# Kernel tuning notes

Hardware: AMD Instinct MI355X
Metric: run time of the kernel (lower is better)

Reference implementation:

```python
import jax, jax.numpy as jnp
import numpy as np

D_MODEL = 2048
NUM_EXPERTS = 64
TOP_K = 2


def setup_inputs() -> dict:
    key = jax.random.key(0)
    kx, kw, kb = jax.random.split(key, 3)
    x = jax.random.normal(kx, (4, 4096, D_MODEL), dtype=jnp.float32)
    # nn.Linear(d_model, num_experts): weight [num_experts, d_model], bias [num_experts]
    bound = 1.0 / np.sqrt(D_MODEL)
    W = jax.random.uniform(kw, (NUM_EXPERTS, D_MODEL), minval=-bound, maxval=bound, dtype=jnp.float32)
    b = jax.random.uniform(kb, (NUM_EXPERTS,), minval=-bound, maxval=bound, dtype=jnp.float32)
    return {"x": x, "W": W, "b": b}


def reference(x, W, b):
    # Eval mode: no noise injection (self.training is False).
    logits = jnp.einsum('bsd,ed->bse', x, W) + b          # [B, S, E]
    raw_weights = jax.nn.softmax(logits, axis=-1)          # [B, S, E]
    top_k_weights, top_k_indices = jax.lax.top_k(raw_weights, TOP_K)  # [B, S, K]
    normalized = top_k_weights / jnp.sum(top_k_weights, axis=-1, keepdims=True)
    return normalized, top_k_indices
```

## Files before the change

kernel.cpp:

```cpp
#include <hip/hip_runtime.h>
#include <math.h>

#define DM 2048
#define NEXP 64
#define NTOK 16384
#define NSLICE 4
#define KSL (DM / NSLICE)
#define KC 32
#define NCH (KSL / KC)
#define MBLK 64
#define NBLK1 ((NTOK / MBLK) * NSLICE)
#define NKG (DM / KC)
#define WFRAG_BYTES (NKG * 12 * 1024)
#define PART_BYTES (NSLICE * NEXP * NTOK * 4)

typedef __attribute__((ext_vector_type(8))) short short8;
typedef __attribute__((ext_vector_type(4))) short short4v;
typedef __attribute__((ext_vector_type(4))) float f32x4;

__device__ __forceinline__ void split3t(float f, unsigned short& h,
                                        unsigned short& m, unsigned short& l) {
  unsigned u = __float_as_uint(f);
  h = (unsigned short)(u >> 16);
  float f1 = f - __uint_as_float(u & 0xFFFF0000u);
  unsigned u1 = __float_as_uint(f1);
  m = (unsigned short)(u1 >> 16);
  float f2 = f1 - __uint_as_float(u1 & 0xFFFF0000u);
  l = (unsigned short)(__float_as_uint(f2) >> 16);
}

__device__ __forceinline__ void split8(const f32x4& a0, const f32x4& a1,
                                       short8& h, short8& m, short8& l) {
  float v[8] = {a0[0], a0[1], a0[2], a0[3], a1[0], a1[1], a1[2], a1[3]};
#pragma unroll
  for (int j = 0; j < 8; ++j) {
    unsigned short hh, mm, ll;
    split3t(v[j], hh, mm, ll);
    h[j] = (short)hh; m[j] = (short)mm; l[j] = (short)ll;
  }
}

__global__ void convw_kernel(const float* __restrict__ W,
                             unsigned short* __restrict__ wfrag) {
  const int kg = blockIdx.x;
  const int lane = threadIdx.x & 63;
  const int nt = threadIdx.x >> 6;
  const int e = nt * 16 + (lane & 15);
  const int kpos = kg * 32 + (lane >> 4) * 8;
  const f32x4* wp = (const f32x4*)(W + (size_t)e * DM + kpos);
  f32x4 w0 = wp[0], w1 = wp[1];
  short8 h, m, l;
  split8(w0, w1, h, m, l);
  size_t base = ((size_t)(kg * 12 + nt) * 64 + lane) * 8;
  *(short8*)(wfrag + base) = h;
  *(short8*)(wfrag + base + (size_t)4 * 64 * 8) = m;
  *(short8*)(wfrag + base + (size_t)8 * 64 * 8) = l;
}

__global__ __launch_bounds__(256, 4)
void router_gemm(const float* __restrict__ x,
                 const unsigned short* __restrict__ wfrag,
                 float* __restrict__ part) {
  const int lane = threadIdx.x & 63;
  const int wv = threadIdx.x >> 6;
  const int col = lane & 15;
  const int quad = lane >> 4;
  const int tg = blockIdx.x >> 2;
  const int s = blockIdx.x & 3;
  const int tok0 = tg * MBLK;
  const int kg0 = s * NCH;

  const float* xp =
      x + (size_t)(tok0 + wv * 16 + col) * DM + s * KSL + quad * 8;
  const unsigned short* bb = wfrag + (size_t)lane * 8;

  f32x4 acc[4];
#pragma unroll
  for (int nt = 0; nt < 4; ++nt) acc[nt] = (f32x4){0.f, 0.f, 0.f, 0.f};

  f32x4 pa0 = ((const f32x4*)xp)[0];
  f32x4 pa1 = ((const f32x4*)xp)[1];
  f32x4 qa0 = ((const f32x4*)(xp + KC))[0];
  f32x4 qa1 = ((const f32x4*)(xp + KC))[1];

  short8 Bh = *(const short8*)(bb + (size_t)(kg0 * 12 + 0) * 512);
  short8 Bm = *(const short8*)(bb + (size_t)(kg0 * 12 + 4) * 512);
  short8 Bl = *(const short8*)(bb + (size_t)(kg0 * 12 + 8) * 512);

#pragma unroll
  for (int c = 0; c < NCH; ++c) {
    const int kg = kg0 + c;
    short8 ah, am, al;
    split8(pa0, pa1, ah, am, al);
    pa0 = qa0; pa1 = qa1;
    if (c + 2 < NCH) {
      const float* xn = xp + (size_t)(c + 2) * KC;
      qa0 = ((const f32x4*)xn)[0];
      qa1 = ((const f32x4*)xn)[1];
    }
#pragma unroll
    for (int nt = 0; nt < 4; ++nt) {
      short8 bh = Bh, bm = Bm, bl = Bl;
      const int nf = (nt < 3) ? (kg * 12 + nt + 1)
                              : ((c + 1 < NCH) ? (kg + 1) * 12 : -1);
      if (nf >= 0) {
        Bh = *(const short8*)(bb + (size_t)(nf + 0) * 512);
        Bm = *(const short8*)(bb + (size_t)(nf + 4) * 512);
        Bl = *(const short8*)(bb + (size_t)(nf + 8) * 512);
      }
      f32x4 cc = acc[nt];
      cc = __builtin_amdgcn_mfma_f32_16x16x32_bf16(ah, bh, cc, 0, 0, 0);
      cc = __builtin_amdgcn_mfma_f32_16x16x32_bf16(ah, bm, cc, 0, 0, 0);
      cc = __builtin_amdgcn_mfma_f32_16x16x32_bf16(am, bh, cc, 0, 0, 0);
      cc = __builtin_amdgcn_mfma_f32_16x16x32_bf16(ah, bl, cc, 0, 0, 0);
      cc = __builtin_amdgcn_mfma_f32_16x16x32_bf16(al, bh, cc, 0, 0, 0);
      cc = __builtin_amdgcn_mfma_f32_16x16x32_bf16(am, bm, cc, 0, 0, 0);
      acc[nt] = cc;
    }
  }

#pragma unroll
  for (int nt = 0; nt < 4; ++nt) {
    const size_t e = (size_t)(s * NEXP + nt * 16 + col);
    *(f32x4*)(part + e * NTOK + tok0 + wv * 16 + quad * 4) = acc[nt];
  }
}

__global__ __launch_bounds__(256, 4)
void router_reduce(const float* __restrict__ part,
                   const float* __restrict__ bias, float* __restrict__ out) {
  const int lane = threadIdx.x & 63;
  const int wv = threadIdx.x >> 6;
  const int q = lane >> 4;
  const int t = blockIdx.x * 64 + wv * 16 + (lane & 15);

  float v1 = -INFINITY, v2 = -INFINITY;
  int i1 = 0, i2 = 0;
#pragma unroll
  for (int e = 0; e < NEXP; ++e) {
    float p = part[(size_t)(q * NEXP + e) * NTOK + t];
    p += __shfl_xor(p, 16, 64);
    p += __shfl_xor(p, 32, 64);
    const float v = p + bias[e];
    const bool a = v > v1;
    const bool b = v > v2;
    const float nv2 = a ? v1 : (b ? v : v2);
    const int ni2 = a ? i1 : (b ? e : i2);
    v2 = nv2; i2 = ni2;
    i1 = a ? e : i1;
    v1 = a ? v : v1;
  }
  if (q == 0) {
    const float ex = expf(v2 - v1);
    const float den = 1.f + ex;
    *(float2*)(out + 2 * t) = make_float2(1.f / den, ex / den);
    *(float2*)(out + 2 * NTOK + 2 * t) = make_float2((float)i1, (float)i2);
  }
}

__global__ __launch_bounds__(512, 2)
void router_fb(const float* __restrict__ x, const float* __restrict__ W,
               const float* __restrict__ bias, float* __restrict__ out) {
  const int lane = threadIdx.x & 63;
  const int wv = threadIdx.x >> 6;
  const int col = lane & 15;
  const int quad = lane >> 4;
  const int tok0 = blockIdx.x * 32;
  const int k0 = wv * 256;

  __shared__ float part[8][32][68];

  f32x4 acc[2][4];
#pragma unroll
  for (int ms = 0; ms < 2; ++ms)
#pragma unroll
    for (int nt = 0; nt < 4; ++nt) acc[ms][nt] = (f32x4){0.f, 0.f, 0.f, 0.f};

  for (int ks = 0; ks < 8; ++ks) {
    const int k = k0 + ks * 32 + quad * 8;
    short8 ah[2], am2[2], al2[2];
#pragma unroll
    for (int ms = 0; ms < 2; ++ms) {
      const f32x4* ap = (const f32x4*)(x + (size_t)(tok0 + ms * 16 + col) * DM + k);
      f32x4 a0 = ap[0], a1 = ap[1];
      split8(a0, a1, ah[ms], am2[ms], al2[ms]);
    }
#pragma unroll
    for (int nt = 0; nt < 4; ++nt) {
      short8 bh, bm, bl;
      const f32x4* wp = (const f32x4*)(W + (size_t)(nt * 16 + col) * DM + k);
      f32x4 w0 = wp[0], w1 = wp[1];
      split8(w0, w1, bh, bm, bl);
#pragma unroll
      for (int ms = 0; ms < 2; ++ms) {
        f32x4 cc = acc[ms][nt];
        cc = __builtin_amdgcn_mfma_f32_16x16x32_bf16(ah[ms], bh, cc, 0, 0, 0);
        cc = __builtin_amdgcn_mfma_f32_16x16x32_bf16(ah[ms], bm, cc, 0, 0, 0);
        cc = __builtin_amdgcn_mfma_f32_16x16x32_bf16(am2[ms], bh, cc, 0, 0, 0);
        cc = __builtin_amdgcn_mfma_f32_16x16x32_bf16(ah[ms], bl, cc, 0, 0, 0);
        cc = __builtin_amdgcn_mfma_f32_16x16x32_bf16(al2[ms], bh, cc, 0, 0, 0);
        cc = __builtin_amdgcn_mfma_f32_16x16x32_bf16(am2[ms], bm, cc, 0, 0, 0);
        acc[ms][nt] = cc;
      }
    }
  }
#pragma unroll
  for (int ms = 0; ms < 2; ++ms)
#pragma unroll
    for (int nt = 0; nt < 4; ++nt)
#pragma unroll
      for (int r = 0; r < 4; ++r)
        part[wv][ms * 16 + quad * 4 + r][nt * 16 + col] = acc[ms][nt][r];
  __syncthreads();
  const float bl_ = bias[lane];
#pragma unroll
  for (int ti = 0; ti < 4; ++ti) {
    const int t = wv * 4 + ti;
    float v1 = bl_;
#pragma unroll
    for (int p = 0; p < 8; ++p) v1 += part[p][t][lane];
    int i1 = lane;
    float v2 = -INFINITY;
    int i2 = NEXP;
#pragma unroll
    for (int off = 32; off > 0; off >>= 1) {
      float ov1 = __shfl_xor(v1, off, 64);
      int   oi1 = __shfl_xor(i1, off, 64);
      float ov2 = __shfl_xor(v2, off, 64);
      int   oi2 = __shfl_xor(i2, off, 64);
      bool afirst = (v1 > ov1) || (v1 == ov1 && i1 < oi1);
      float w1v = afirst ? v1 : ov1;  int w1i = afirst ? i1 : oi1;
      float c1v = afirst ? v2 : ov2;  int c1i = afirst ? i2 : oi2;
      float c2v = afirst ? ov1 : v1;  int c2i = afirst ? oi1 : i1;
      bool sfirst = (c1v > c2v) || (c1v == c2v && c1i < c2i);
      v1 = w1v; i1 = w1i;
      v2 = sfirst ? c1v : c2v;
      i2 = sfirst ? c1i : c2i;
    }
    if (lane == 0) {
      const float ex = expf(v2 - v1);
      const float den = 1.f + ex;
      const int token = tok0 + t;
      *(float2*)(out + 2 * token) = make_float2(1.f / den, ex / den);
      *(float2*)(out + 2 * NTOK + 2 * token) =
          make_float2((float)i1, (float)i2);
    }
  }
}

extern "C" void kernel_launch(void* const* d_in, const int* in_sizes, int n_in,
                              void* d_out, int out_size, void* d_ws, size_t ws_size,
                              hipStream_t stream) {
  const float* x = (const float*)d_in[0];
  const float* W = (const float*)d_in[1];
  const float* b = (const float*)d_in[2];
  float* out = (float*)d_out;

  const size_t need = (size_t)WFRAG_BYTES + (size_t)PART_BYTES;
  if (ws_size >= need) {
    unsigned short* wfrag = (unsigned short*)d_ws;
    float* part = (float*)((char*)d_ws + WFRAG_BYTES);
    hipLaunchKernelGGL(convw_kernel, dim3(NKG), dim3(256), 0, stream, W, wfrag);
    hipLaunchKernelGGL(router_gemm, dim3(NBLK1), dim3(256), 0, stream,
                       x, wfrag, part);
    hipLaunchKernelGGL(router_reduce, dim3(NTOK / 64), dim3(256), 0, stream,
                       part, b, out);
  } else {
    hipLaunchKernelGGL(router_fb, dim3(NTOK / 32), dim3(512), 0, stream,
                       x, W, b, out);
  }
}
```

Measured before the change: 221.9 us.

## Fuse split-K router GEMM and top-2 reduction into one kernel via LDS

Replaces the two-kernel path (split-K GEMM writing partial logits to global memory, then a separate reduce/top-2 kernel) with a single kernel. Each block now covers 32 tokens, and its four waves split K four ways, so each wave reuses every weight fragment across two 16-token M-tiles. Partial sums go to shared memory and two waves finish the K reduction, bias add, top-2 selection and renormalisation. This removes the large partial-logit round trip through HBM and one launch, at the cost of fewer blocks, higher register pressure and an unconditional weight prefetch that reads past the fragment buffer into the padded workspace.

```diff
diff --git a/kernel.cpp b/kernel.cpp
--- a/kernel.cpp
+++ b/kernel.cpp
@@ -4,15 +4,14 @@
 #define DM 2048
 #define NEXP 64
 #define NTOK 16384
-#define NSLICE 4
-#define KSL (DM / NSLICE)
 #define KC 32
+#define KSL 512
 #define NCH (KSL / KC)
-#define MBLK 64
-#define NBLK1 ((NTOK / MBLK) * NSLICE)
+#define MBLK 32
+#define NBLK (NTOK / MBLK)
 #define NKG (DM / KC)
 #define WFRAG_BYTES (NKG * 12 * 1024)
-#define PART_BYTES (NSLICE * NEXP * NTOK * 4)
+#define QS 2120
 
 typedef __attribute__((ext_vector_type(8))) short short8;
 typedef __attribute__((ext_vector_type(4))) short short4v;
@@ -57,104 +56,118 @@
   *(short8*)(wfrag + base + (size_t)8 * 64 * 8) = l;
 }
 
-__global__ __launch_bounds__(256, 4)
-void router_gemm(const float* __restrict__ x,
-                 const unsigned short* __restrict__ wfrag,
-                 float* __restrict__ part) {
+__global__ __launch_bounds__(256, 2)
+void router_fused(const float* __restrict__ x,
+                  const unsigned short* __restrict__ wfrag,
+                  const float* __restrict__ bias, float* __restrict__ out) {
   const int lane = threadIdx.x & 63;
   const int wv = threadIdx.x >> 6;
   const int col = lane & 15;
   const int quad = lane >> 4;
-  const int tg = blockIdx.x >> 2;
-  const int s = blockIdx.x & 3;
-  const int tok0 = tg * MBLK;
-  const int kg0 = s * NCH;
-
-  const float* xp =
-      x + (size_t)(tok0 + wv * 16 + col) * DM + s * KSL + quad * 8;
+  const int tok0 = blockIdx.x * MBLK;
+  const int kg0 = wv * NCH;
+
+  __shared__ float pl[4 * QS];
+
+  const float* xp0 = x + (size_t)(tok0 + col) * DM + wv * KSL + quad * 8;
+  const float* xp1 = xp0 + (size_t)16 * DM;
   const unsigned short* bb = wfrag + (size_t)lane * 8;
 
-  f32x4 acc[4];
-#pragma unroll
-  for (int nt = 0; nt < 4; ++nt) acc[nt] = (f32x4){0.f, 0.f, 0.f, 0.f};
-
-  f32x4 pa0 = ((const f32x4*)xp)[0];
-  f32x4 pa1 = ((const f32x4*)xp)[1];
-  f32x4 qa0 = ((const f32x4*)(xp + KC))[0];
-  f32x4 qa1 = ((const f32x4*)(xp + KC))[1];
+  f32x4 acc[2][4];
+#pragma unroll
+  for (int mt = 0; mt < 2; ++mt)
+#pragma unroll
+    for (int nt = 0; nt < 4; ++nt) acc[mt][nt] = (f32x4){0.f, 0.f, 0.f, 0.f};
+
+  f32x4 P00 = ((const f32x4*)xp0)[0], P01 = ((const f32x4*)xp0)[1];
+  f32x4 P10 = ((const f32x4*)xp1)[0], P11 = ((const f32x4*)xp1)[1];
+  f32x4 Q00 = ((const f32x4*)(xp0 + KC))[0], Q01 = ((const f32x4*)(xp0 + KC))[1];
+  f32x4 Q10 = ((const f32x4*)(xp1 + KC))[0], Q11 = ((const f32x4*)(xp1 + KC))[1];
 
   short8 Bh = *(const short8*)(bb + (size_t)(kg0 * 12 + 0) * 512);
   short8 Bm = *(const short8*)(bb + (size_t)(kg0 * 12 + 4) * 512);
   short8 Bl = *(const short8*)(bb + (size_t)(kg0 * 12 + 8) * 512);
 
-#pragma unroll
+#pragma unroll 2
   for (int c = 0; c < NCH; ++c) {
     const int kg = kg0 + c;
-    short8 ah, am, al;
-    split8(pa0, pa1, ah, am, al);
-    pa0 = qa0; pa1 = qa1;
+    short8 ah0, am0, al0, ah1, am1, al1;
+    split8(P00, P01, ah0, am0, al0);
+    split8(P10, P11, ah1, am1, al1);
+    P00 = Q00; P01 = Q01; P10 = Q10; P11 = Q11;
     if (c + 2 < NCH) {
-      const float* xn = xp + (size_t)(c + 2) * KC;
-      qa0 = ((const f32x4*)xn)[0];
-      qa1 = ((const f32x4*)xn)[1];
+      const float* n0 = xp0 + (size_t)(c + 2) * KC;
+      const float* n1 = xp1 + (size_t)(c + 2) * KC;
+      Q00 = ((const f32x4*)n0)[0]; Q01 = ((const f32x4*)n0)[1];
+      Q10 = ((const f32x4*)n1)[0]; Q11 = ((const f32x4*)n1)[1];
     }
 #pragma unroll
     for (int nt = 0; nt < 4; ++nt) {
       short8 bh = Bh, bm = Bm, bl = Bl;
-      const int nf = (nt < 3) ? (kg * 12 + nt + 1)
-                              : ((c + 1 < NCH) ? (kg + 1) * 12 : -1);
-      if (nf >= 0) {
-        Bh = *(const short8*)(bb + (size_t)(nf + 0) * 512);
-        Bm = *(const short8*)(bb + (size_t)(nf + 4) * 512);
-        Bl = *(const short8*)(bb + (size_t)(nf + 8) * 512);
+      const int nf = (nt < 3) ? (kg * 12 + nt + 1) : (kg + 1) * 12;
+      Bh = *(const short8*)(bb + (size_t)(nf + 0) * 512);
+      Bm = *(const short8*)(bb + (size_t)(nf + 4) * 512);
+      Bl = *(const short8*)(bb + (size_t)(nf + 8) * 512);
+      {
+        f32x4 cc = acc[0][nt];
+        cc = __builtin_amdgcn_mfma_f32_16x16x32_bf16(ah0, bh, cc, 0, 0, 0);
+        cc = __builtin_amdgcn_mfma_f32_16x16x32_bf16(ah0, bm, cc, 0, 0, 0);
+        cc = __builtin_amdgcn_mfma_f32_16x16x32_bf16(am0, bh, cc, 0, 0, 0);
+        cc = __builtin_amdgcn_mfma_f32_16x16x32_bf16(ah0, bl, cc, 0, 0, 0);
+        cc = __builtin_amdgcn_mfma_f32_16x16x32_bf16(al0, bh, cc, 0, 0, 0);
+        cc = __builtin_amdgcn_mfma_f32_16x16x32_bf16(am0, bm, cc, 0, 0, 0);
+        acc[0][nt] = cc;
       }
-      f32x4 cc = acc[nt];
-      cc = __builtin_amdgcn_mfma_f32_16x16x32_bf16(ah, bh, cc, 0, 0, 0);
-      cc = __builtin_amdgcn_mfma_f32_16x16x32_bf16(ah, bm, cc, 0, 0, 0);
-      cc = __builtin_amdgcn_mfma_f32_16x16x32_bf16(am, bh, cc, 0, 0, 0);
-      cc = __builtin_amdgcn_mfma_f32_16x16x32_bf16(ah, bl, cc, 0, 0, 0);
-      cc = __builtin_amdgcn_mfma_f32_16x16x32_bf16(al, bh, cc, 0, 0, 0);
-      cc = __builtin_amdgcn_mfma_f32_16x16x32_bf16(am, bm, cc, 0, 0, 0);
-      acc[nt] = cc;
-    }
-  }
-
-#pragma unroll
-  for (int nt = 0; nt < 4; ++nt) {
-    const size_t e = (size_t)(s * NEXP + nt * 16 + col);
-    *(f32x4*)(part + e * NTOK + tok0 + wv * 16 + quad * 4) = acc[nt];
-  }
-}
-
-__global__ __launch_bounds__(256, 4)
-void router_reduce(const float* __restrict__ part,
-                   const float* __restrict__ bias, float* __restrict__ out) {
-  const int lane = threadIdx.x & 63;
-  const int wv = threadIdx.x >> 6;
-  const int q = lane >> 4;
-  const int t = blockIdx.x * 64 + wv * 16 + (lane & 15);
-
-  float v1 = -INFINITY, v2 = -INFINITY;
-  int i1 = 0, i2 = 0;
-#pragma unroll
-  for (int e = 0; e < NEXP; ++e) {
-    float p = part[(size_t)(q * NEXP + e) * NTOK + t];
-    p += __shfl_xor(p, 16, 64);
-    p += __shfl_xor(p, 32, 64);
-    const float v = p + bias[e];
-    const bool a = v > v1;
-    const bool b = v > v2;
-    const float nv2 = a ? v1 : (b ? v : v2);
-    const int ni2 = a ? i1 : (b ? e : i2);
-    v2 = nv2; i2 = ni2;
-    i1 = a ? e : i1;
-    v1 = a ? v : v1;
-  }
-  if (q == 0) {
-    const float ex = expf(v2 - v1);
-    const float den = 1.f + ex;
-    *(float2*)(out + 2 * t) = make_float2(1.f / den, ex / den);
-    *(float2*)(out + 2 * NTOK + 2 * t) = make_float2((float)i1, (float)i2);
+      {
+        f32x4 cc = acc[1][nt];
+        cc = __builtin_amdgcn_mfma_f32_16x16x32_bf16(ah1, bh, cc, 0, 0, 0);
+        cc = __builtin_amdgcn_mfma_f32_16x16x32_bf16(ah1, bm, cc, 0, 0, 0);
+        cc = __builtin_amdgcn_mfma_f32_16x16x32_bf16(am1, bh, cc, 0, 0, 0);
+        cc = __builtin_amdgcn_mfma_f32_16x16x32_bf16(ah1, bl, cc, 0, 0, 0);
+        cc = __builtin_amdgcn_mfma_f32_16x16x32_bf16(al1, bh, cc, 0, 0, 0);
+        cc = __builtin_amdgcn_mfma_f32_16x16x32_bf16(am1, bm, cc, 0, 0, 0);
+        acc[1][nt] = cc;
+      }
+    }
+  }
+
+#pragma unroll
+  for (int mt = 0; mt < 2; ++mt)
+#pragma unroll
+    for (int nt = 0; nt < 4; ++nt)
+#pragma unroll
+      for (int r = 0; r < 4; ++r)
+        pl[wv * QS + (mt * 16 + quad * 4 + r) * 66 + nt * 16 + col] =
+            acc[mt][nt][r];
+  __syncthreads();
+
+  if (wv < 2) {
+    const int tt = lane & 15;
+    const int q = lane >> 4;
+    const int tl = wv * 16 + tt;
+    float v1 = -INFINITY, v2 = -INFINITY;
+    int i1 = 0, i2 = 0;
+#pragma unroll
+    for (int e = 0; e < NEXP; ++e) {
+      float p = pl[q * QS + tl * 66 + e];
+      p += __shfl_xor(p, 16, 64);
+      p += __shfl_xor(p, 32, 64);
+      const float v = p + bias[e];
+      const bool a = v > v1;
+      const bool b = v > v2;
+      const float nv2 = a ? v1 : (b ? v : v2);
+      const int ni2 = a ? i1 : (b ? e : i2);
+      v2 = nv2; i2 = ni2;
+      i1 = a ? e : i1;
+      v1 = a ? v : v1;
+    }
+    if (q == 0) {
+      const int t = tok0 + tl;
+      const float ex = expf(v2 - v1);
+      const float den = 1.f + ex;
+      *(float2*)(out + 2 * t) = make_float2(1.f / den, ex / den);
+      *(float2*)(out + 2 * NTOK + 2 * t) = make_float2((float)i1, (float)i2);
+    }
   }
 }
 
@@ -256,15 +269,12 @@
   const float* b = (const float*)d_in[2];
   float* out = (float*)d_out;
 
-  const size_t need = (size_t)WFRAG_BYTES + (size_t)PART_BYTES;
+  const size_t need = (size_t)WFRAG_BYTES + 16384;
   if (ws_size >= need) {
     unsigned short* wfrag = (unsigned short*)d_ws;
-    float* part = (float*)((char*)d_ws + WFRAG_BYTES);
     hipLaunchKernelGGL(convw_kernel, dim3(NKG), dim3(256), 0, stream, W, wfrag);
-    hipLaunchKernelGGL(router_gemm, dim3(NBLK1), dim3(256), 0, stream,
-                       x, wfrag, part);
-    hipLaunchKernelGGL(router_reduce, dim3(NTOK / 64), dim3(256), 0, stream,
-                       part, b, out);
+    hipLaunchKernelGGL(router_fused, dim3(NBLK), dim3(256), 0, stream,
+                       x, wfrag, b, out);
   } else {
     hipLaunchKernelGGL(router_fb, dim3(NTOK / 32), dim3(512), 0, stream,
                        x, W, b, out);
```

Measured after the change: 210.0 us. 1.06x faster.
